# Kernel optimization log

Hardware: AMD Instinct MI355X
Metric: run time of the kernel (lower is better)

Reference implementation:

```python
import jax, jax.numpy as jnp
import numpy as np

C = 128        # in_channels
HEADS = 4
B, D, H, W = 4, 16, 64, 64  # H must equal W for this module's matmul to type-check


def conv1x1(x, Wm, b):
    # 1x1x1 Conv3d == per-voxel linear over channels
    return jnp.einsum('bcdhw,oc->bodhw', x, Wm) + b[None, :, None, None, None]


def setup_inputs() -> dict:
    key = jax.random.key(0)
    ks = jax.random.split(key, 14)
    scale = 1.0 / np.sqrt(C)

    def wmat(k):
        return jax.random.normal(k, (C, C), jnp.float32) * scale

    def bvec(k):
        return jax.random.normal(k, (C,), jnp.float32) * 0.01

    return {
        'x':  jax.random.normal(ks[0], (B, C, D, H, W), jnp.float32),
        'Wq': wmat(ks[1]),  'bq': bvec(ks[2]),
        'Wk': wmat(ks[3]),  'bk': bvec(ks[4]),
        'Wv': wmat(ks[5]),  'bv': bvec(ks[6]),
        'Wa1': wmat(ks[7]), 'ba1': bvec(ks[8]),
        'Wa2': wmat(ks[9]), 'ba2': bvec(ks[10]),
        'Wf': wmat(ks[11]), 'bf': bvec(ks[12]),
    }


def reference(x, Wq, bq, Wk, bk, Wv, bv, Wa1, ba1, Wa2, ba2, Wf, bf):
    b, c, d, h, w = x.shape
    ch = c // HEADS  # channels per head

    q = conv1x1(x, Wq, bq).reshape(b, HEADS, ch, d, h, w)
    k = conv1x1(x, Wk, bk).reshape(b, HEADS, ch, d, h, w)
    v = conv1x1(x, Wv, bv).reshape(b, HEADS, ch, d, h, w)

    # attention over the last spatial axis: (W, H)^T @ (H, W) -> (W, W)
    attn = jnp.einsum('bhcdxi,bhcdxj->bhcdij', q, k)  # [b, heads, ch, d, W, W]
    attn = jax.nn.softmax(attn, axis=-1)
    # (W, W) @ (H=W, W) -> (W, W)
    out = jnp.einsum('bhcdik,bhcdkj->bhcdij', attn, v)
    out = out.reshape(b, c, d, h, w)

    # depth=1 attention layer: conv1x1 -> relu -> conv1x1
    out = conv1x1(jax.nn.relu(conv1x1(out, Wa1, ba1)), Wa2, ba2)
    out = conv1x1(out, Wf, bf)
    return out
```

## Files before the change

kernel.cpp:

```cpp
#include <hip/hip_runtime.h>


#define CCH 128
#define SPB 65536
#define NBATCH 4
#define WTAB 16384

typedef float f32x4 __attribute__((ext_vector_type(4)));
typedef __bf16 bf16x8 __attribute__((ext_vector_type(8)));
typedef short s16x8 __attribute__((ext_vector_type(8)));
typedef unsigned short u16x8 __attribute__((ext_vector_type(8)));
typedef unsigned short u16x4 __attribute__((ext_vector_type(4)));
typedef unsigned int u32x2 __attribute__((ext_vector_type(2)));

template <typename T>
static __device__ __forceinline__ auto mfma_try(T a, T b, f32x4 c, int)
    -> decltype(__builtin_amdgcn_mfma_f32_16x16x32_bf16(a, b, c, 0, 0, 0)) {
  return __builtin_amdgcn_mfma_f32_16x16x32_bf16(a, b, c, 0, 0, 0);
}
template <typename T>
static __device__ __forceinline__ f32x4 mfma_try(T a, T b, f32x4 c, long) {
  return __builtin_amdgcn_mfma_f32_16x16x32_bf16(
      __builtin_bit_cast(bf16x8, a), __builtin_bit_cast(bf16x8, b), c, 0, 0, 0);
}
static __device__ __forceinline__ f32x4 MFMA16(u16x8 a, u16x8 b, f32x4 c) {
  return mfma_try(__builtin_bit_cast(s16x8, a), __builtin_bit_cast(s16x8, b), c, 0);
}

static __device__ __forceinline__ unsigned short f2b(float f) {
  return __builtin_bit_cast(unsigned short, (__bf16)f);
}
static __device__ __forceinline__ unsigned int pk2(float a, float b) {
  return (unsigned int)f2b(a) | ((unsigned int)f2b(b) << 16);
}

static __device__ __forceinline__ void glds16(const unsigned short* g,
                                              unsigned short* l) {
  __builtin_amdgcn_global_load_lds(
      (const __attribute__((address_space(1))) unsigned int*)g,
      (__attribute__((address_space(3))) unsigned int*)l, 16, 0, 0);
}

static __device__ __forceinline__ void bar_lgkm() {
  asm volatile("s_waitcnt lgkmcnt(0)" ::: "memory");
  __builtin_amdgcn_sched_barrier(0);
  __builtin_amdgcn_s_barrier();
  __builtin_amdgcn_sched_barrier(0);
}
static __device__ __forceinline__ void bar_vm0() {
  asm volatile("s_waitcnt vmcnt(0)" ::: "memory");
  __builtin_amdgcn_sched_barrier(0);
  __builtin_amdgcn_s_barrier();
  __builtin_amdgcn_sched_barrier(0);
}
static __device__ __forceinline__ void bar_vm16() {
  asm volatile("s_waitcnt vmcnt(16)" ::: "memory");
  __builtin_amdgcn_sched_barrier(0);
  __builtin_amdgcn_s_barrier();
  __builtin_amdgcn_sched_barrier(0);
}

static __device__ __forceinline__ int swzc(int r, int c) {
  int slot = ((c >> 3) ^ (r & 7) ^ ((r >> 3) & 15)) & 15;
  return r * 128 + slot * 8 + (c & 7);
}
static __device__ __forceinline__ int widx(int r, int c) {
  return (r & 64) * 128 + swzc(r & 63, c);
}
static __device__ __forceinline__ int swat(int w, int x) {
  int slot = ((x >> 3) ^ (w & 7) ^ ((w >> 3) & 7)) & 7;
  return w * 64 + slot * 8 + (x & 7);
}
static __device__ __forceinline__ int pix(int i, int j) {
  int slot = ((j >> 3) ^ (((i >> 2) & 3) << 1)) & 7;
  return i * 64 + slot * 8 + (j & 7);
}

__global__ __launch_bounds__(256) void prep_w_kernel(
    const float* __restrict__ Wq, const float* __restrict__ Wk,
    const float* __restrict__ Wv, const float* __restrict__ W1,
    const float* __restrict__ W2, const float* __restrict__ W3,
    unsigned short* __restrict__ out)
{
  const float* Ws[6] = {Wq, Wk, Wv, W1, W2, W3};
  const float* W = Ws[blockIdx.x];
  unsigned short* o = out + (size_t)blockIdx.x * WTAB;
  const int tid = threadIdx.x;
#pragma unroll
  for (int p = 0; p < 16; ++p) {
    const int base = p * 1024 + tid * 4;
    const int m = base >> 7;
    const int c0 = base & 127;
    f32x4 v = *(const f32x4*)&W[base];
    u16x4 u;
#pragma unroll
    for (int e = 0; e < 4; ++e) u[e] = f2b(v[e]);
    *(u16x4*)&o[widx(m, c0)] = u;
  }
}

__global__ __launch_bounds__(256, 3) void qkv_kernel(
    const float* __restrict__ X, const unsigned short* __restrict__ Wbf,
    const float* __restrict__ Bq, const float* __restrict__ Bk,
    const float* __restrict__ Bv,
    unsigned short* __restrict__ Yq, unsigned short* __restrict__ Yk,
    unsigned short* __restrict__ Yv)
{
  __shared__ unsigned short xc[16384];
  __shared__ unsigned short wb[8192];
  __shared__ float bias_lds[3][128];

  const int tid  = threadIdx.x;
  const int wv   = tid >> 6;
  const int lane = tid & 63;
  const int lr   = lane & 15;
  const int lg   = lane >> 4;
  const int s0   = blockIdx.x * 128;
  const size_t xbase = (size_t)blockIdx.y * CCH * SPB;
  const int go = tid * 8;

  if (tid < 128) {
    bias_lds[0][tid] = Bq[tid];
    bias_lds[1][tid] = Bk[tid];
    bias_lds[2][tid] = Bv[tid];
  }

  {
    const int cp = tid >> 2;
    const int sq = tid & 3;
    const float* xa = X + xbase + (size_t)(2 * cp) * SPB + s0 + sq * 32;
    const float* xb = xa + SPB;
    unsigned int* xc32 = (unsigned int*)xc;
#pragma unroll
    for (int i = 0; i < 8; ++i) {
      f32x4 a = *(const f32x4*)&xa[4 * i];
      f32x4 b = *(const f32x4*)&xb[4 * i];
#pragma unroll
      for (int e = 0; e < 4; ++e)
        xc32[swzc(sq * 32 + 4 * i + e, 2 * cp) >> 1] = pk2(a[e], b[e]);
    }
  }
  __syncthreads();

  u16x8 afr[2][4];
#pragma unroll
  for (int sf = 0; sf < 2; ++sf)
#pragma unroll
    for (int ks = 0; ks < 4; ++ks)
      afr[sf][ks] = *(const u16x8*)&xc[swzc(wv * 32 + sf * 16 + lr, ks * 32 + lg * 8)];
  __syncthreads();

#pragma unroll
  for (int p = 0; p < 4; ++p) glds16(&Wbf[p * 2048 + go], &wb[p * 2048 + go]);
#pragma unroll
  for (int p = 0; p < 4; ++p) glds16(&Wbf[8192 + p * 2048 + go], &xc[p * 2048 + go]);
  __syncthreads();

#pragma unroll
  for (int ci = 0; ci < 3; ++ci) {
    f32x4 acc[2][8];
#pragma unroll
    for (int sf = 0; sf < 2; ++sf)
#pragma unroll
      for (int of = 0; of < 8; ++of) {
        f32x4 z = {0.f, 0.f, 0.f, 0.f};
        acc[sf][of] = z;
      }
#pragma unroll
    for (int ks = 0; ks < 4; ++ks) {
      const int k0 = ks * 32 + lg * 8;
#pragma unroll
      for (int of = 0; of < 8; ++of) {
        u16x8 bfr = (of < 4)
            ? *(const u16x8*)&wb[swzc(of * 16 + lr, k0)]
            : *(const u16x8*)&xc[swzc((of - 4) * 16 + lr, k0)];
        acc[0][of] = MFMA16(afr[0][ks], bfr, acc[0][of]);
        acc[1][of] = MFMA16(afr[1][ks], bfr, acc[1][of]);
      }
    }

    if (ci < 2) {
      bar_lgkm();
      const unsigned short* Wn = Wbf + (size_t)(ci + 1) * WTAB;
#pragma unroll
      for (int p = 0; p < 4; ++p) glds16(&Wn[p * 2048 + go], &wb[p * 2048 + go]);
#pragma unroll
      for (int p = 0; p < 4; ++p) glds16(&Wn[8192 + p * 2048 + go], &xc[p * 2048 + go]);
      __builtin_amdgcn_sched_barrier(0);
    }

    float bv8[8];
#pragma unroll
    for (int of = 0; of < 8; ++of) bv8[of] = bias_lds[ci][of * 16 + lr];
    unsigned short* Y = (ci == 0) ? Yq : (ci == 1) ? Yk : Yv;
    const int sb = s0 + wv * 32 + lg * 4;
#pragma unroll
    for (int sf = 0; sf < 2; ++sf)
#pragma unroll
      for (int of = 0; of < 8; ++of) {
        u32x2 pk;
        pk.x = pk2(acc[sf][of][0] + bv8[of], acc[sf][of][1] + bv8[of]);
        pk.y = pk2(acc[sf][of][2] + bv8[of], acc[sf][of][3] + bv8[of]);
        *(u32x2*)&Y[xbase + (size_t)(of * 16 + lr) * SPB + sb + sf * 16] = pk;
      }

    if (ci < 2) bar_vm16();
  }
}

__global__ __launch_bounds__(256, 4) void attn64_kernel(
    const unsigned short* __restrict__ Q,
    const unsigned short* __restrict__ K,
    const unsigned short* __restrict__ V,
    unsigned short* __restrict__ O)
{
  __shared__ unsigned short qt[4096];
  __shared__ unsigned short kt[4096];
  __shared__ unsigned short vt[4096];
  __shared__ unsigned short pbuf[4096];

  const int tid  = threadIdx.x;
  const int wv   = tid >> 6;
  const int lane = tid & 63;
  const int lr   = lane & 15;
  const int lg   = lane >> 4;
  const size_t base = (size_t)blockIdx.x * 4096;

  {
    const int x0 = (tid >> 3) * 2;
    const int w0 = (tid & 7) * 8;
    const size_t ga = base + (size_t)x0 * 64 + w0;
    u16x8 qa = *(const u16x8*)&Q[ga], qb = *(const u16x8*)&Q[ga + 64];
    u16x8 ka = *(const u16x8*)&K[ga], kb = *(const u16x8*)&K[ga + 64];
    u16x8 va = *(const u16x8*)&V[ga], vb = *(const u16x8*)&V[ga + 64];
    unsigned int* qt32 = (unsigned int*)qt;
    unsigned int* kt32 = (unsigned int*)kt;
    unsigned int* vt32 = (unsigned int*)vt;
#pragma unroll
    for (int e = 0; e < 8; ++e) {
      const int idx = swat(w0 + e, x0) >> 1;
      qt32[idx] = (unsigned int)qa[e] | ((unsigned int)qb[e] << 16);
      kt32[idx] = (unsigned int)ka[e] | ((unsigned int)kb[e] << 16);
      vt32[idx] = (unsigned int)va[e] | ((unsigned int)vb[e] << 16);
    }
  }
  __syncthreads();

  f32x4 sacc[4];
#pragma unroll
  for (int nf = 0; nf < 4; ++nf) { f32x4 z = {0.f, 0.f, 0.f, 0.f}; sacc[nf] = z; }
#pragma unroll
  for (int ks = 0; ks < 2; ++ks) {
    const int k0 = ks * 32 + lg * 8;
    u16x8 a = *(const u16x8*)&qt[swat(wv * 16 + lr, k0)];
#pragma unroll
    for (int nf = 0; nf < 4; ++nf) {
      u16x8 bb = *(const u16x8*)&kt[swat(nf * 16 + lr, k0)];
      sacc[nf] = MFMA16(a, bb, sacc[nf]);
    }
  }

#pragma unroll
  for (int r = 0; r < 4; ++r) {
    float m = fmaxf(fmaxf(sacc[0][r], sacc[1][r]), fmaxf(sacc[2][r], sacc[3][r]));
    m = fmaxf(m, __shfl_xor(m, 1));
    m = fmaxf(m, __shfl_xor(m, 2));
    m = fmaxf(m, __shfl_xor(m, 4));
    m = fmaxf(m, __shfl_xor(m, 8));
    float sum = 0.f;
#pragma unroll
    for (int nf = 0; nf < 4; ++nf) {
      float p = __expf(sacc[nf][r] - m);
      sacc[nf][r] = p;
      sum += p;
    }
    sum += __shfl_xor(sum, 1);
    sum += __shfl_xor(sum, 2);
    sum += __shfl_xor(sum, 4);
    sum += __shfl_xor(sum, 8);
    const float inv = 1.f / sum;
    const int i = wv * 16 + lg * 4 + r;
#pragma unroll
    for (int nf = 0; nf < 4; ++nf)
      pbuf[pix(i, nf * 16 + lr)] = f2b(sacc[nf][r] * inv);
  }

  f32x4 oacc[4];
#pragma unroll
  for (int nf = 0; nf < 4; ++nf) { f32x4 z = {0.f, 0.f, 0.f, 0.f}; oacc[nf] = z; }
#pragma unroll
  for (int ks = 0; ks < 2; ++ks) {
    const int k0 = ks * 32 + lg * 8;
    u16x8 a = *(const u16x8*)&pbuf[pix(wv * 16 + lr, k0)];
#pragma unroll
    for (int nf = 0; nf < 4; ++nf) {
      u16x8 bb = *(const u16x8*)&vt[swat(nf * 16 + lr, k0)];
      oacc[nf] = MFMA16(bb, a, oacc[nf]);
    }
  }

  {
    const size_t ib = base + (size_t)(16 * wv + lr) * 64 + lg * 4;
#pragma unroll
    for (int nf = 0; nf < 4; ++nf) {
      u32x2 pk;
      pk.x = pk2(oacc[nf][0], oacc[nf][1]);
      pk.y = pk2(oacc[nf][2], oacc[nf][3]);
      *(u32x2*)&O[ib + nf * 16] = pk;
    }
  }
}

__global__ __launch_bounds__(256, 2) void tail_kernel(
    const unsigned short* __restrict__ Xb, const unsigned short* __restrict__ Wbf,
    const float* __restrict__ B1, const float* __restrict__ B2,
    const float* __restrict__ B3, float* __restrict__ OUT)
{
  __shared__ unsigned short wl[16384];
  __shared__ unsigned short xc[16384];
  __shared__ float bias_lds[3][128];

  const int tid  = threadIdx.x;
  const int wv   = tid >> 6;
  const int lane = tid & 63;
  const int lr   = lane & 15;
  const int lg   = lane >> 4;
  const int s0   = blockIdx.x * 128;
  const size_t xbase = (size_t)blockIdx.y * CCH * SPB;
  const int go = tid * 8;

#pragma unroll
  for (int p = 0; p < 8; ++p) glds16(&Wbf[p * 2048 + go], &wl[p * 2048 + go]);

  if (tid < 128) {
    bias_lds[0][tid] = B1[tid];
    bias_lds[1][tid] = B2[tid];
    bias_lds[2][tid] = B3[tid];
  }

  {
    const int cp = tid >> 2;
    const int sq = tid & 3;
    const unsigned short* xa = Xb + xbase + (size_t)(2 * cp) * SPB + s0 + sq * 32;
    const unsigned short* xb = xa + SPB;
    unsigned int* xc32 = (unsigned int*)xc;
#pragma unroll
    for (int i = 0; i < 4; ++i) {
      u16x8 a = *(const u16x8*)&xa[8 * i];
      u16x8 b = *(const u16x8*)&xb[8 * i];
#pragma unroll
      for (int e = 0; e < 8; ++e)
        xc32[swzc(sq * 32 + 8 * i + e, 2 * cp) >> 1] =
            (unsigned int)a[e] | ((unsigned int)b[e] << 16);
    }
  }
  __syncthreads();

  u16x8 bfr[2][4];
#pragma unroll
  for (int nf = 0; nf < 2; ++nf)
#pragma unroll
    for (int ks = 0; ks < 4; ++ks)
      bfr[nf][ks] = *(const u16x8*)&xc[swzc(wv * 32 + nf * 16 + lr, ks * 32 + lg * 8)];

  f32x4 acc[8][2];
  auto gemm_std = [&]() {
#pragma unroll
    for (int mf = 0; mf < 8; ++mf)
#pragma unroll
      for (int nf = 0; nf < 2; ++nf) {
        f32x4 z = {0.f, 0.f, 0.f, 0.f};
        acc[mf][nf] = z;
      }
#pragma unroll
    for (int ks = 0; ks < 4; ++ks) {
      const int k0 = ks * 32 + lg * 8;
#pragma unroll
      for (int mf = 0; mf < 8; ++mf) {
        u16x8 afr = *(const u16x8*)&wl[widx(mf * 16 + lr, k0)];
        acc[mf][0] = MFMA16(afr, bfr[0][ks], acc[mf][0]);
        acc[mf][1] = MFMA16(afr, bfr[1][ks], acc[mf][1]);
      }
    }
  };

  auto epi_chain = [&](int ci, bool relu) {
#pragma unroll
    for (int mf = 0; mf < 8; ++mf)
#pragma unroll
      for (int nf = 0; nf < 2; ++nf) {
        const int s = wv * 32 + nf * 16 + lr;
        const int c0 = mf * 16 + lg * 4;
        f32x4 bb = *(const f32x4*)&bias_lds[ci][c0];
        float v0 = acc[mf][nf][0] + bb[0];
        float v1 = acc[mf][nf][1] + bb[1];
        float v2 = acc[mf][nf][2] + bb[2];
        float v3 = acc[mf][nf][3] + bb[3];
        if (relu) {
          v0 = fmaxf(v0, 0.f); v1 = fmaxf(v1, 0.f);
          v2 = fmaxf(v2, 0.f); v3 = fmaxf(v3, 0.f);
        }
        u32x2 pk;
        pk.x = pk2(v0, v1);
        pk.y = pk2(v2, v3);
        *(u32x2*)&xc[swzc(s, c0)] = pk;
      }
#pragma unroll
    for (int nf = 0; nf < 2; ++nf)
#pragma unroll
      for (int ks = 0; ks < 4; ++ks)
        bfr[nf][ks] = *(const u16x8*)&xc[swzc(wv * 32 + nf * 16 + lr, ks * 32 + lg * 8)];
  };

#pragma unroll
  for (int j = 0; j < 2; ++j) {
    gemm_std();
    bar_lgkm();
    const unsigned short* Wn = Wbf + (size_t)(j + 1) * WTAB;
#pragma unroll
    for (int p = 0; p < 8; ++p) glds16(&Wn[p * 2048 + go], &wl[p * 2048 + go]);
    epi_chain(j, j == 0);
    bar_vm0();
  }

  {
    f32x4 acc3[2][8];
#pragma unroll
    for (int sf = 0; sf < 2; ++sf)
#pragma unroll
      for (int of = 0; of < 8; ++of) {
        f32x4 z = {0.f, 0.f, 0.f, 0.f};
        acc3[sf][of] = z;
      }
#pragma unroll
    for (int ks = 0; ks < 4; ++ks) {
      const int k0 = ks * 32 + lg * 8;
#pragma unroll
      for (int of = 0; of < 8; ++of) {
        u16x8 wfr = *(const u16x8*)&wl[widx(of * 16 + lr, k0)];
        acc3[0][of] = MFMA16(bfr[0][ks], wfr, acc3[0][of]);
        acc3[1][of] = MFMA16(bfr[1][ks], wfr, acc3[1][of]);
      }
    }
    const int sb = s0 + wv * 32 + lg * 4;
#pragma unroll
    for (int sf = 0; sf < 2; ++sf)
#pragma unroll
      for (int of = 0; of < 8; ++of) {
        const float b = bias_lds[2][of * 16 + lr];
        f32x4 v = acc3[sf][of];
        v[0] += b; v[1] += b; v[2] += b; v[3] += b;
        *(f32x4*)&OUT[xbase + (size_t)(of * 16 + lr) * SPB + sb + sf * 16] = v;
      }
  }
}

extern "C" void kernel_launch(void* const* d_in, const int* in_sizes, int n_in,
                              void* d_out, int out_size, void* d_ws, size_t ws_size,
                              hipStream_t stream) {
  const float* x   = (const float*)d_in[0];
  const float* Wq  = (const float*)d_in[1];  const float* bq  = (const float*)d_in[2];
  const float* Wk  = (const float*)d_in[3];  const float* bk  = (const float*)d_in[4];
  const float* Wv  = (const float*)d_in[5];  const float* bv  = (const float*)d_in[6];
  const float* Wa1 = (const float*)d_in[7];  const float* ba1 = (const float*)d_in[8];
  const float* Wa2 = (const float*)d_in[9];  const float* ba2 = (const float*)d_in[10];
  const float* Wf  = (const float*)d_in[11]; const float* bf_ = (const float*)d_in[12];

  unsigned short* qb  = (unsigned short*)d_ws;
  unsigned short* wbf = qb + (size_t)NBATCH * CCH * SPB;
  unsigned short* kb = (unsigned short*)d_out;
  unsigned short* vb = kb + (size_t)NBATCH * CCH * SPB;

  dim3 grid(SPB / 128, NBATCH);

  prep_w_kernel<<<6, 256, 0, stream>>>(Wq, Wk, Wv, Wa1, Wa2, Wf, wbf);

  qkv_kernel<<<grid, 256, 0, stream>>>(x, wbf, bq, bk, bv, qb, kb, vb);

  attn64_kernel<<<NBATCH * CCH * 16, 256, 0, stream>>>(qb, kb, vb, qb);

  tail_kernel<<<grid, 256, 0, stream>>>(qb, wbf + (size_t)3 * WTAB,
                                        ba1, ba2, bf_, (float*)d_out);
}
```

Measured before the change: 219.0 us.

## Restructure QKV projection: resident weights, LDS-staged coalesced stores, prefetched X tiles

The QKV kernel now uses 512-thread blocks that each cover 512 spatial positions in four 128-wide sub-tiles. All three bf16 weight tables stay resident in LDS for the whole block, so they are no longer reloaded per output. The next X sub-tile is prefetched into registers while the current one is being computed. Each projection result is staged through a swizzled LDS buffer and written out as 16-byte coalesced row stores, replacing the scattered 8-byte stores. In exchange, LDS use per block rises, occupancy drops to two blocks, and more barriers are added per sub-tile.

Result: faster. 177.3 us (-19.0%).

```diff
diff --git a/kernel.cpp b/kernel.cpp
--- a/kernel.cpp
+++ b/kernel.cpp
@@ -53,12 +53,6 @@
   __builtin_amdgcn_s_barrier();
   __builtin_amdgcn_sched_barrier(0);
 }
-static __device__ __forceinline__ void bar_vm16() {
-  asm volatile("s_waitcnt vmcnt(16)" ::: "memory");
-  __builtin_amdgcn_sched_barrier(0);
-  __builtin_amdgcn_s_barrier();
-  __builtin_amdgcn_sched_barrier(0);
-}
 
 static __device__ __forceinline__ int swzc(int r, int c) {
   int slot = ((c >> 3) ^ (r & 7) ^ ((r >> 3) & 15)) & 15;
@@ -66,6 +60,10 @@
 }
 static __device__ __forceinline__ int widx(int r, int c) {
   return (r & 64) * 128 + swzc(r & 63, c);
+}
+static __device__ __forceinline__ int cbix(int o, int s) {
+  int slot = ((s >> 3) ^ (o & 15)) & 15;
+  return o * 128 + slot * 8 + (s & 7);
 }
 static __device__ __forceinline__ int swat(int w, int x) {
   int slot = ((x >> 3) ^ (w & 7) ^ ((w >> 3) & 7)) & 7;
@@ -99,112 +97,123 @@
   }
 }
 
-__global__ __launch_bounds__(256, 3) void qkv_kernel(
+__global__ __launch_bounds__(512, 2) void qkv_kernel(
     const float* __restrict__ X, const unsigned short* __restrict__ Wbf,
     const float* __restrict__ Bq, const float* __restrict__ Bk,
     const float* __restrict__ Bv,
     unsigned short* __restrict__ Yq, unsigned short* __restrict__ Yk,
     unsigned short* __restrict__ Yv)
 {
-  __shared__ unsigned short xc[16384];
-  __shared__ unsigned short wb[8192];
-  __shared__ float bias_lds[3][128];
+  __shared__ unsigned short wt[3 * WTAB];
+  __shared__ unsigned short xb[WTAB];
 
   const int tid  = threadIdx.x;
   const int wv   = tid >> 6;
   const int lane = tid & 63;
   const int lr   = lane & 15;
   const int lg   = lane >> 4;
-  const int s0   = blockIdx.x * 128;
-  const size_t xbase = (size_t)blockIdx.y * CCH * SPB;
+  const int sbase = blockIdx.x * 512;
+  const size_t xoff = (size_t)blockIdx.y * CCH * SPB;
+
   const int go = tid * 8;
-
-  if (tid < 128) {
-    bias_lds[0][tid] = Bq[tid];
-    bias_lds[1][tid] = Bk[tid];
-    bias_lds[2][tid] = Bv[tid];
-  }
-
-  {
-    const int cp = tid >> 2;
-    const int sq = tid & 3;
-    const float* xa = X + xbase + (size_t)(2 * cp) * SPB + s0 + sq * 32;
-    const float* xb = xa + SPB;
-    unsigned int* xc32 = (unsigned int*)xc;
-#pragma unroll
-    for (int i = 0; i < 8; ++i) {
-      f32x4 a = *(const f32x4*)&xa[4 * i];
-      f32x4 b = *(const f32x4*)&xb[4 * i];
-#pragma unroll
-      for (int e = 0; e < 4; ++e)
-        xc32[swzc(sq * 32 + 4 * i + e, 2 * cp) >> 1] = pk2(a[e], b[e]);
-    }
-  }
+#pragma unroll
+  for (int t = 0; t < 3; ++t)
+#pragma unroll
+    for (int p = 0; p < 4; ++p)
+      glds16(&Wbf[t * WTAB + p * 4096 + go], &wt[t * WTAB + p * 4096 + go]);
+
+  float bq_v[8], bk_v[8], bv_v[8];
+#pragma unroll
+  for (int of = 0; of < 8; ++of) {
+    bq_v[of] = Bq[of * 16 + lr];
+    bk_v[of] = Bk[of * 16 + lr];
+    bv_v[of] = Bv[of * 16 + lr];
+  }
+
+  const int c0  = (tid >> 3) * 2;
+  const int sb8 = (tid & 7) * 4;
+  const float* xrow = X + xoff + (size_t)c0 * SPB + sbase;
+  unsigned int* xb32 = (unsigned int*)xb;
+
+  f32x4 xr[8];
+#pragma unroll
+  for (int i = 0; i < 4; ++i) {
+    xr[i]     = *(const f32x4*)&xrow[sb8 + 32 * i];
+    xr[4 + i] = *(const f32x4*)&xrow[SPB + sb8 + 32 * i];
+  }
+#pragma unroll
+  for (int i = 0; i < 4; ++i)
+#pragma unroll
+    for (int e = 0; e < 4; ++e)
+      xb32[swzc(sb8 + 32 * i + e, c0) >> 1] = pk2(xr[i][e], xr[4 + i][e]);
   __syncthreads();
 
-  u16x8 afr[2][4];
-#pragma unroll
-  for (int sf = 0; sf < 2; ++sf)
+#pragma unroll
+  for (int si = 0; si < 4; ++si) {
+    const int sg = sbase + si * 128;
+
+    u16x8 afr[4];
 #pragma unroll
     for (int ks = 0; ks < 4; ++ks)
-      afr[sf][ks] = *(const u16x8*)&xc[swzc(wv * 32 + sf * 16 + lr, ks * 32 + lg * 8)];
-  __syncthreads();
-
-#pragma unroll
-  for (int p = 0; p < 4; ++p) glds16(&Wbf[p * 2048 + go], &wb[p * 2048 + go]);
-#pragma unroll
-  for (int p = 0; p < 4; ++p) glds16(&Wbf[8192 + p * 2048 + go], &xc[p * 2048 + go]);
-  __syncthreads();
-
-#pragma unroll
-  for (int ci = 0; ci < 3; ++ci) {
-    f32x4 acc[2][8];
-#pragma unroll
-    for (int sf = 0; sf < 2; ++sf)
+      afr[ks] = *(const u16x8*)&xb[swzc(wv * 16 + lr, ks * 32 + lg * 8)];
+
+    if (si < 3) {
+      const float* xn = xrow + (si + 1) * 128;
+#pragma unroll
+      for (int i = 0; i < 4; ++i) {
+        xr[i]     = *(const f32x4*)&xn[sb8 + 32 * i];
+        xr[4 + i] = *(const f32x4*)&xn[SPB + sb8 + 32 * i];
+      }
+    }
+    bar_lgkm();
+
+    auto conv = [&](int t, const float (&b8)[8], unsigned short* __restrict__ Y) {
+      f32x4 acc[8];
 #pragma unroll
       for (int of = 0; of < 8; ++of) {
         f32x4 z = {0.f, 0.f, 0.f, 0.f};
-        acc[sf][of] = z;
-      }
-#pragma unroll
-    for (int ks = 0; ks < 4; ++ks) {
-      const int k0 = ks * 32 + lg * 8;
+        acc[of] = z;
+      }
+#pragma unroll
+      for (int ks = 0; ks < 4; ++ks) {
+        const int k0 = ks * 32 + lg * 8;
+#pragma unroll
+        for (int of = 0; of < 8; ++of) {
+          u16x8 wfr = *(const u16x8*)&wt[t * WTAB + widx(of * 16 + lr, k0)];
+          acc[of] = MFMA16(afr[ks], wfr, acc[of]);
+        }
+      }
 #pragma unroll
       for (int of = 0; of < 8; ++of) {
-        u16x8 bfr = (of < 4)
-            ? *(const u16x8*)&wb[swzc(of * 16 + lr, k0)]
-            : *(const u16x8*)&xc[swzc((of - 4) * 16 + lr, k0)];
-        acc[0][of] = MFMA16(afr[0][ks], bfr, acc[0][of]);
-        acc[1][of] = MFMA16(afr[1][ks], bfr, acc[1][of]);
-      }
-    }
-
-    if (ci < 2) {
+        const float b = b8[of];
+        u32x2 pk;
+        pk.x = pk2(acc[of][0] + b, acc[of][1] + b);
+        pk.y = pk2(acc[of][2] + b, acc[of][3] + b);
+        *(u32x2*)&xb[cbix(of * 16 + lr, wv * 16 + lg * 4)] = pk;
+      }
       bar_lgkm();
-      const unsigned short* Wn = Wbf + (size_t)(ci + 1) * WTAB;
-#pragma unroll
-      for (int p = 0; p < 4; ++p) glds16(&Wn[p * 2048 + go], &wb[p * 2048 + go]);
-#pragma unroll
-      for (int p = 0; p < 4; ++p) glds16(&Wn[8192 + p * 2048 + go], &xc[p * 2048 + go]);
-      __builtin_amdgcn_sched_barrier(0);
-    }
-
-    float bv8[8];
-#pragma unroll
-    for (int of = 0; of < 8; ++of) bv8[of] = bias_lds[ci][of * 16 + lr];
-    unsigned short* Y = (ci == 0) ? Yq : (ci == 1) ? Yk : Yv;
-    const int sb = s0 + wv * 32 + lg * 4;
-#pragma unroll
-    for (int sf = 0; sf < 2; ++sf)
-#pragma unroll
-      for (int of = 0; of < 8; ++of) {
-        u32x2 pk;
-        pk.x = pk2(acc[sf][of][0] + bv8[of], acc[sf][of][1] + bv8[of]);
-        pk.y = pk2(acc[sf][of][2] + bv8[of], acc[sf][of][3] + bv8[of]);
-        *(u32x2*)&Y[xbase + (size_t)(of * 16 + lr) * SPB + sb + sf * 16] = pk;
-      }
-
-    if (ci < 2) bar_vm16();
+#pragma unroll
+      for (int p = 0; p < 4; ++p) {
+        const int row = p * 32 + (tid >> 4);
+        const int sc  = (tid & 15) * 8;
+        u16x8 v = *(const u16x8*)&xb[cbix(row, sc)];
+        *(u16x8*)&Y[xoff + (size_t)row * SPB + sg + sc] = v;
+      }
+      bar_lgkm();
+    };
+
+    conv(0, bq_v, Yq);
+    conv(1, bk_v, Yk);
+    conv(2, bv_v, Yv);
+
+    if (si < 3) {
+#pragma unroll
+      for (int i = 0; i < 4; ++i)
+#pragma unroll
+        for (int e = 0; e < 4; ++e)
+          xb32[swzc(sb8 + 32 * i + e, c0) >> 1] = pk2(xr[i][e], xr[4 + i][e]);
+      __syncthreads();
+    }
   }
 }
 
@@ -471,14 +480,13 @@
   unsigned short* kb = (unsigned short*)d_out;
   unsigned short* vb = kb + (size_t)NBATCH * CCH * SPB;
 
-  dim3 grid(SPB / 128, NBATCH);
-
   prep_w_kernel<<<6, 256, 0, stream>>>(Wq, Wk, Wv, Wa1, Wa2, Wf, wbf);
 
-  qkv_kernel<<<grid, 256, 0, stream>>>(x, wbf, bq, bk, bv, qb, kb, vb);
+  qkv_kernel<<<dim3(SPB / 512, NBATCH), 512, 0, stream>>>(
+      x, wbf, bq, bk, bv, qb, kb, vb);
 
   attn64_kernel<<<NBATCH * CCH * 16, 256, 0, stream>>>(qb, kb, vb, qb);
 
-  tail_kernel<<<grid, 256, 0, stream>>>(qb, wbf + (size_t)3 * WTAB,
-                                        ba1, ba2, bf_, (float*)d_out);
-}
+  tail_kernel<<<dim3(SPB / 128, NBATCH), 256, 0, stream>>>(
+      qb, wbf + (size_t)3 * WTAB, ba1, ba2, bf_, (float*)d_out);
+}
```
